# Performance work log

Measured on AMD Instinct MI355X. Metric: run time of the kernel, lower is better.

Reference implementation:

```python
import jax, jax.numpy as jnp
import numpy as np
import math

B, S, H = 2, 2048, 4096
NH, HD, KVH = 32, 128, 8
GROUPS = NH // KVH  # repeat_kv n_rep
BASE = 10000.0
TRAINING_SEQLEN = 8192
BASE_SEQLEN = 8192


def _rope_cos_sin(s):
    # RotaryEmbedding.forward: seq_len = max(s, training_seqlen); NTK-alpha scaled base; mscale
    seq_len = max(s, TRAINING_SEQLEN)
    context_value = math.log(seq_len / BASE_SEQLEN, 2) + 1
    ntk_alpha = max(2 ** math.ceil(context_value) - 1, 1)
    scale = seq_len / TRAINING_SEQLEN
    mscale = 1.0 if scale <= 1 else 0.1 * math.log(scale) + 1.0
    base = BASE * ntk_alpha ** (HD / (HD - 2))
    inv_freq = 1.0 / base ** (np.arange(0, HD, 2, dtype=np.float32) / HD)
    t = np.arange(seq_len, dtype=np.float32)
    freqs = np.outer(t, inv_freq)          # [seq_len, HD/2]
    emb = np.concatenate([freqs, freqs], axis=-1)  # [seq_len, HD]
    return jnp.asarray(mscale * np.cos(emb)[:s]), jnp.asarray(mscale * np.sin(emb)[:s])


def _rotate_half(x):
    x1, x2 = jnp.split(x, 2, axis=-1)
    return jnp.concatenate([-x2, x1], axis=-1)


def setup_inputs() -> dict:
    key = jax.random.key(0)
    ks = jax.random.split(key, 5)
    hidden_states = jax.random.normal(ks[0], (B, S, H), jnp.float32)
    residual = jax.random.normal(ks[1], (B, S, H), jnp.float32)
    causal = jnp.triu(jnp.ones((S, S), dtype=bool), k=1)  # True = masked (masked_fill semantics)
    attention_mask = jnp.broadcast_to(causal[None, None], (B, 1, S, S))
    W_q = jax.random.normal(ks[2], (H, H), jnp.float32) / np.float32(np.sqrt(H))
    W_kv = jax.random.normal(ks[3], (H, 2 * KVH * HD), jnp.float32) / np.float32(np.sqrt(H))
    W_dense = jax.random.normal(ks[4], (H, H), jnp.float32) / np.float32(np.sqrt(H))
    b_dense = jnp.zeros((H,), jnp.float32)
    return dict(hidden_states=hidden_states, residual=residual, attention_mask=attention_mask,
                W_q=W_q, W_kv=W_kv, W_dense=W_dense, b_dense=b_dense)


def reference(hidden_states, residual, attention_mask, W_q, W_kv, W_dense, b_dense):
    # QKV projections (Linear, no bias for query/key_value)
    q = (hidden_states @ W_q).reshape(B, S, NH, HD)            # [B,S,NH,HD]
    kvp = (hidden_states @ W_kv).reshape(B, S, KVH, 2 * HD)
    k, v = kvp[..., :HD], kvp[..., HD:]                        # [B,S,KVH,HD]
    # rotary (NTK-scaled), applied identically to q and k
    cos, sin = _rope_cos_sin(S)
    cos = cos[None, :, None, :]
    sin = sin[None, :, None, :]
    q = q * cos + _rotate_half(q) * sin
    k = k * cos + _rotate_half(k) * sin
    # repeat_kv: each kv head repeated GROUPS times consecutively
    k = jnp.repeat(k, GROUPS, axis=2)                          # [B,S,NH,HD]
    v = jnp.repeat(v, GROUPS, axis=2)
    # scaled dot-product attention with causal mask
    scores = jnp.einsum('bqhd,bkhd->bhqk', q, k) * (1.0 / np.float32(np.sqrt(HD)))
    scores = jnp.where(attention_mask, jnp.finfo(scores.dtype).min, scores)
    probs = jax.nn.softmax(scores, axis=-1)                    # attention_dropout=0 (eval)
    ctx = jnp.einsum('bhqk,bkhd->bqhd', probs, v).reshape(B, S, H)
    # dense (with bias) + dropout_add residual (dropout inactive in eval)
    out = ctx @ W_dense + b_dense
    return residual + out
```

## Files before the change

kernel.cpp:

```cpp
#include <hip/hip_runtime.h>
#include <hip/hip_bf16.h>


#define BB   2
#define SS   2048
#define HH   4096
#define NHH  32
#define HDD  128
#define KVHH 8

typedef unsigned short u16;
typedef __attribute__((ext_vector_type(8))) short  short8;
typedef __attribute__((ext_vector_type(4))) float  floatx4;

#define AS1 __attribute__((address_space(1)))
#define AS3 __attribute__((address_space(3)))

__device__ __forceinline__ void gll16(const void* g, void* l) {
    __builtin_amdgcn_global_load_lds((const AS1 unsigned int*)g,
                                     (AS3 unsigned int*)l, 16, 0, 0);
}
__device__ __forceinline__ float b2f(u16 x) {
    union { unsigned int u; float f; } c; c.u = ((unsigned int)x) << 16; return c.f;
}
__device__ __forceinline__ u16 f2b(float f) {
    union { float f; unsigned int u; } c; c.f = f;
    unsigned int r = 0x7FFFu + ((c.u >> 16) & 1u);
    return (u16)((c.u + r) >> 16);
}

__global__ __launch_bounds__(256)
void cvt_kernel(const float* __restrict__ X, u16* __restrict__ Y, int n4) {
    int i = blockIdx.x * 256 + threadIdx.x;
    if (i >= n4) return;
    float4 v = *(const float4*)(X + (size_t)i * 4);
    size_t o = (size_t)i * 4;
    Y[o + 0] = f2b(v.x); Y[o + 1] = f2b(v.y);
    Y[o + 2] = f2b(v.z); Y[o + 3] = f2b(v.w);
}

__global__ __launch_bounds__(256) void rope_table(float* __restrict__ ct,
                                                  float* __restrict__ st) {
    int idx = blockIdx.x * 256 + threadIdx.x;
    if (idx >= SS * 64) return;
    int s = idx >> 6, i = idx & 63;
    double inv = pow(10000.0, -(double)(2 * i) / 128.0);
    double f = (double)s * inv;
    ct[idx] = (float)cos(f);
    st[idx] = (float)sin(f);
}

__global__ __launch_bounds__(256) void wt_kernel(const float* __restrict__ W,
                                                 u16* __restrict__ WT,
                                                 int R, int C) {
    __shared__ u16 t[64 * 65];
    int tcols = C >> 6;
    int ty = blockIdx.x / tcols, tx = blockIdx.x % tcols;
    int r0 = ty * 64, c0 = tx * 64;
    for (int idx = threadIdx.x; idx < 4096; idx += 256) {
        int r = idx >> 6, c = idx & 63;
        t[r * 65 + c] = f2b(W[(size_t)(r0 + r) * C + c0 + c]);
    }
    __syncthreads();
    for (int idx = threadIdx.x; idx < 4096; idx += 256) {
        int c = idx >> 6, r = idx & 63;
        WT[(size_t)(c0 + c) * R + r0 + r] = t[r * 65 + c];
    }
}

__global__ __launch_bounds__(256, 2)
void gemm_bt(const u16* __restrict__ A, const u16* __restrict__ BT,
             u16* __restrict__ C, float* __restrict__ Cf,
             int M, int N, int K,
             const float* __restrict__ bias, const float* __restrict__ resid) {
    __shared__ u16 sA[128 * 32];
    __shared__ u16 sB[128 * 32];
    const int tid = threadIdx.x;
    const int wave = tid >> 6, lane = tid & 63;
    const int m0 = blockIdx.y * 128, n0 = blockIdx.x * 128;
    const int wm = (wave >> 1) * 64, wn = (wave & 1) * 64;
    const int srow = lane >> 2, scol = (lane & 3) * 8;
    const int frow = lane & 15, fquad = lane >> 4;
    const int fk = fquad * 8;

    const floatx4 fz = {0.f, 0.f, 0.f, 0.f};
    floatx4 acc[4][4];
#pragma unroll
    for (int i = 0; i < 4; ++i)
#pragma unroll
        for (int j = 0; j < 4; ++j) acc[i][j] = fz;

    for (int kt = 0; kt < K; kt += 32) {
#pragma unroll
        for (int j = 0; j < 2; ++j) {
            int rb = (wave + j * 4) * 16;
            gll16(A  + (size_t)(m0 + rb + srow) * K + kt + scol, &sA[rb * 32]);
            gll16(BT + (size_t)(n0 + rb + srow) * K + kt + scol, &sB[rb * 32]);
        }
        __syncthreads();
        short8 af[4];
#pragma unroll
        for (int i = 0; i < 4; ++i)
            af[i] = *(const short8*)&sA[(wm + i * 16 + frow) * 32 + fk];
#pragma unroll
        for (int jn = 0; jn < 4; ++jn) {
            short8 bfr = *(const short8*)&sB[(wn + jn * 16 + frow) * 32 + fk];
#pragma unroll
            for (int i = 0; i < 4; ++i)
                acc[i][jn] = __builtin_amdgcn_mfma_f32_16x16x32_bf16(
                    af[i], bfr, acc[i][jn], 0, 0, 0);
        }
        __syncthreads();
    }
#pragma unroll
    for (int i = 0; i < 4; ++i) {
#pragma unroll
        for (int jn = 0; jn < 4; ++jn) {
            int col = n0 + wn + jn * 16 + frow;
            float bv = bias ? bias[col] : 0.f;
#pragma unroll
            for (int r = 0; r < 4; ++r) {
                int row = m0 + wm + i * 16 + fquad * 4 + r;
                float v = acc[i][jn][r] + bv;
                if (Cf) {
                    if (resid) v += resid[(size_t)row * N + col];
                    Cf[(size_t)row * N + col] = v;
                } else {
                    C[(size_t)row * N + col] = f2b(v);
                }
            }
        }
    }
}

__global__ __launch_bounds__(256)
void rope_apply(u16* __restrict__ Qb, u16* __restrict__ KVb,
                const float* __restrict__ ct, const float* __restrict__ st) {
    int gid = blockIdx.x * 256 + threadIdx.x;
    int row = gid >> 6, d = gid & 63;
    const int nq = BB * SS * NHH;
    u16* p;
    int s;
    if (row < nq) {
        s = (row / NHH) % SS;
        p = Qb + (size_t)row * HDD;
    } else {
        int r2 = row - nq;
        s = (r2 / KVHH) % SS;
        p = KVb + (size_t)r2 * 256;
    }
    float c = ct[s * 64 + d], sn = st[s * 64 + d];
    float x0 = b2f(p[d]), x1 = b2f(p[d + 64]);
    p[d]      = f2b(x0 * c - x1 * sn);
    p[d + 64] = f2b(x1 * c + x0 * sn);
}

__global__ __launch_bounds__(256)
void vt_kernel(const u16* __restrict__ KVb, u16* __restrict__ VT) {
    __shared__ u16 t[64 * 130];
    int bid = blockIdx.x;
    int bk = bid >> 5;
    int s0 = (bid & 31) * 64;
    int b = bk >> 3, kvh = bk & 7;
    for (int idx = threadIdx.x; idx < 64 * 128; idx += 256) {
        int si = idx >> 7, d = idx & 127;
        t[si * 130 + d] =
            KVb[((size_t)((b * SS + s0 + si) * KVHH + kvh)) * 256 + 128 + d];
    }
    __syncthreads();
    for (int idx = threadIdx.x; idx < 64 * 128; idx += 256) {
        int d = idx >> 6, sj = idx & 63;
        VT[((size_t)(bk * HDD + d)) * SS + s0 + sj] = t[sj * 130 + d];
    }
}

__global__ __launch_bounds__(256, 3)
void attn(const u16* __restrict__ Q, const u16* __restrict__ KV,
          const u16* __restrict__ VT, u16* __restrict__ CTX) {
    __shared__ u16 smem[25600];
    u16* sK  = smem;
    u16* sVT = smem + 8192;
    u16* sP  = smem + 16384;

    const int tid = threadIdx.x;
    const int wave = tid >> 6, lane = tid & 63;
    const int frow = lane & 15, fquad = lane >> 4;
    const int bid = blockIdx.x;
    const int qt = 15 - (bid >> 6);
    const int b = (bid >> 5) & 1;
    const int h = bid & 31;
    const int kvh = h >> 2;
    const int q0 = qt * 128;

    {
        const int srow4 = lane >> 4;
        const int chunk = lane & 15;
#pragma unroll
        for (int j = 0; j < 8; ++j) {
            int rb = (j * 4 + wave) * 4;
            int sc = chunk ^ ((rb + srow4) & 7);
            gll16(Q + ((size_t)((b * SS + q0 + rb + srow4) * NHH + h)) * HDD + sc * 8,
                  &smem[rb * 128]);
        }
    }
    __syncthreads();
    short8 qf[2][4];
#pragma unroll
    for (int mi = 0; mi < 2; ++mi)
#pragma unroll
        for (int ds = 0; ds < 4; ++ds)
            qf[mi][ds] = *(const short8*)
                &smem[(wave * 32 + mi * 16 + frow) * 128 +
                      ((ds * 4 + fquad) ^ (frow & 7)) * 8];
    __syncthreads();

    const floatx4 fz = {0.f, 0.f, 0.f, 0.f};
    floatx4 o[2][8];
#pragma unroll
    for (int mi = 0; mi < 2; ++mi)
#pragma unroll
        for (int dn = 0; dn < 8; ++dn) o[mi][dn] = fz;
    float mrow[2][4], lrow[2][4];
#pragma unroll
    for (int mi = 0; mi < 2; ++mi)
#pragma unroll
        for (int r = 0; r < 4; ++r) { mrow[mi][r] = -1e30f; lrow[mi][r] = 0.f; }

    const float scale = 0.08838834764831845f;
    const int nt = 2 * (qt + 1);
    for (int t = 0; t < nt; ++t) {
        const int k0 = t * 64;
        {
            const int srow4 = lane >> 4, ch16 = lane & 15;
#pragma unroll
            for (int j = 0; j < 4; ++j) {
                int rb = (j * 4 + wave) * 4;
                int sc = ch16 ^ ((rb + srow4) & 7);
                gll16(KV + ((size_t)((b * SS + k0 + rb + srow4) * KVHH + kvh)) * 256 + sc * 8,
                      &sK[rb * 128]);
            }
            const int srow8 = lane >> 3, ch8 = lane & 7;
#pragma unroll
            for (int j = 0; j < 4; ++j) {
                int rb = (j * 4 + wave) * 8;
                int sc = ch8 ^ ((rb + srow8) & 7);
                gll16(VT + ((size_t)((b * KVHH + kvh) * HDD + rb + srow8)) * SS + k0 + sc * 8,
                      &sVT[rb * 64]);
            }
        }
        __syncthreads();

        floatx4 sc[2][4];
#pragma unroll
        for (int mi = 0; mi < 2; ++mi)
#pragma unroll
            for (int ni = 0; ni < 4; ++ni) sc[mi][ni] = fz;
#pragma unroll
        for (int ds = 0; ds < 4; ++ds) {
#pragma unroll
            for (int ni = 0; ni < 4; ++ni) {
                short8 kf = *(const short8*)
                    &sK[(ni * 16 + frow) * 128 +
                        ((ds * 4 + fquad) ^ (frow & 7)) * 8];
                sc[0][ni] = __builtin_amdgcn_mfma_f32_16x16x32_bf16(
                    qf[0][ds], kf, sc[0][ni], 0, 0, 0);
                sc[1][ni] = __builtin_amdgcn_mfma_f32_16x16x32_bf16(
                    qf[1][ds], kf, sc[1][ni], 0, 0, 0);
            }
        }

        const bool dgt = (t >= 2 * qt);
#pragma unroll
        for (int mi = 0; mi < 2; ++mi) {
#pragma unroll
            for (int r = 0; r < 4; ++r) {
                int qg = q0 + wave * 32 + mi * 16 + fquad * 4 + r;
                float mx = -1e30f;
#pragma unroll
                for (int ni = 0; ni < 4; ++ni) {
                    float v = sc[mi][ni][r] * scale;
                    if (dgt) {
                        int kg = k0 + ni * 16 + frow;
                        if (kg > qg) v = -1e30f;
                    }
                    sc[mi][ni][r] = v;
                    mx = fmaxf(mx, v);
                }
                mx = fmaxf(mx, __shfl_xor(mx, 1));
                mx = fmaxf(mx, __shfl_xor(mx, 2));
                mx = fmaxf(mx, __shfl_xor(mx, 4));
                mx = fmaxf(mx, __shfl_xor(mx, 8));
                float mold = mrow[mi][r];
                float mnew = fmaxf(mold, mx);
                float alpha = __expf(mold - mnew);
                mrow[mi][r] = mnew;
                float rs = 0.f;
#pragma unroll
                for (int ni = 0; ni < 4; ++ni) {
                    float pv = __expf(sc[mi][ni][r] - mnew);
                    sc[mi][ni][r] = pv;
                    rs += pv;
                }
                rs += __shfl_xor(rs, 1);
                rs += __shfl_xor(rs, 2);
                rs += __shfl_xor(rs, 4);
                rs += __shfl_xor(rs, 8);
                lrow[mi][r] = lrow[mi][r] * alpha + rs;
#pragma unroll
                for (int dn = 0; dn < 8; ++dn) o[mi][dn][r] *= alpha;
            }
        }

#pragma unroll
        for (int mi = 0; mi < 2; ++mi)
#pragma unroll
            for (int ni = 0; ni < 4; ++ni)
#pragma unroll
                for (int r = 0; r < 4; ++r)
                    sP[(wave * 32 + mi * 16 + fquad * 4 + r) * 72 + ni * 16 + frow] =
                        f2b(sc[mi][ni][r]);
        asm volatile("s_waitcnt lgkmcnt(0)" ::: "memory");

#pragma unroll
        for (int ks = 0; ks < 2; ++ks) {
            short8 pf0 = *(const short8*)
                &sP[(wave * 32 + frow) * 72 + ks * 32 + fquad * 8];
            short8 pf1 = *(const short8*)
                &sP[(wave * 32 + 16 + frow) * 72 + ks * 32 + fquad * 8];
#pragma unroll
            for (int dn = 0; dn < 8; ++dn) {
                short8 vf = *(const short8*)
                    &sVT[(dn * 16 + frow) * 64 +
                         ((ks * 4 + fquad) ^ (frow & 7)) * 8];
                o[0][dn] = __builtin_amdgcn_mfma_f32_16x16x32_bf16(pf0, vf, o[0][dn], 0, 0, 0);
                o[1][dn] = __builtin_amdgcn_mfma_f32_16x16x32_bf16(pf1, vf, o[1][dn], 0, 0, 0);
            }
        }
        __syncthreads();
    }

#pragma unroll
    for (int mi = 0; mi < 2; ++mi) {
#pragma unroll
        for (int r = 0; r < 4; ++r) {
            float inv = 1.f / lrow[mi][r];
            int qg = q0 + wave * 32 + mi * 16 + fquad * 4 + r;
            size_t base = ((size_t)(b * SS + qg) * NHH + h) * HDD;
#pragma unroll
            for (int dn = 0; dn < 8; ++dn)
                CTX[base + dn * 16 + frow] = f2b(o[mi][dn][r] * inv);
        }
    }
}

extern "C" void kernel_launch(void* const* d_in, const int* in_sizes, int n_in,
                              void* d_out, int out_size, void* d_ws, size_t ws_size,
                              hipStream_t stream) {
    const float* hidden = (const float*)d_in[0];
    const float* resid  = (const float*)d_in[1];
    const float* Wq  = (const float*)d_in[3];
    const float* Wkv = (const float*)d_in[4];
    const float* Wd  = (const float*)d_in[5];
    const float* bd  = (const float*)d_in[6];
    float* out = (float*)d_out;

    char* ws = (char*)d_ws;
    u16*   hsb = (u16*)(ws);
    u16*   Qb  = (u16*)(ws + ((size_t)32 << 20));
    u16*   KVb = (u16*)(ws + ((size_t)64 << 20));
    u16*   T1  = (u16*)(ws + ((size_t)80 << 20));
    u16*   VTb = (u16*)(ws + ((size_t)112 << 20));
    float* ct  = (float*)(ws + ((size_t)120 << 20));
    float* st  = (float*)(ws + ((size_t)120 << 20) + ((size_t)512 << 10));

    const int M = BB * SS;

    rope_table<<<512, 256, 0, stream>>>(ct, st);
    cvt_kernel<<<(M * HH / 4 + 255) / 256, 256, 0, stream>>>(hidden, hsb, M * HH / 4);

    wt_kernel<<<4096, 256, 0, stream>>>(Wq, T1, HH, HH);
    gemm_bt<<<dim3(32, 32), 256, 0, stream>>>(hsb, T1, Qb, nullptr, M, HH, HH,
                                              nullptr, nullptr);
    wt_kernel<<<2048, 256, 0, stream>>>(Wkv, T1, HH, 2 * KVHH * HDD);
    gemm_bt<<<dim3(16, 32), 256, 0, stream>>>(hsb, T1, KVb, nullptr,
                                              M, 2 * KVHH * HDD, HH,
                                              nullptr, nullptr);

    rope_apply<<<(BB * SS * (NHH + KVHH) * 64) / 256, 256, 0, stream>>>(Qb, KVb, ct, st);
    vt_kernel<<<BB * KVHH * (SS / 64), 256, 0, stream>>>(KVb, VTb);

    attn<<<BB * 16 * NHH, 256, 0, stream>>>(Qb, KVb, VTb, Qb);

    wt_kernel<<<4096, 256, 0, stream>>>(Wd, T1, HH, HH);
    gemm_bt<<<dim3(32, 32), 256, 0, stream>>>(Qb, T1, nullptr, out, M, HH, HH,
                                              bd, resid);
}
```

Before: 984.8 us.

## Register-prefetch K/V tiles in attention, lazy softmax rescale, vectorize rope

The attention loop now prefetches the next K and V^T tiles from global memory into registers while the current tile is computed, replacing the direct global-to-LDS loads. This is meant to hide load latency behind the MFMA work. Softmax rescaling of the output accumulators is skipped unless some row max grows by more than 8, and s_setprio is raised around the MFMA blocks. The rope kernel handles four elements per thread with vector loads and stores. The trade-offs are higher register pressure and an extra register-to-LDS copy per tile.

```diff
diff --git a/kernel.cpp b/kernel.cpp
--- a/kernel.cpp
+++ b/kernel.cpp
@@ -11,6 +11,7 @@
 
 typedef unsigned short u16;
 typedef __attribute__((ext_vector_type(8))) short  short8;
+typedef __attribute__((ext_vector_type(4))) short  short4b;
 typedef __attribute__((ext_vector_type(4))) float  floatx4;
 
 #define AS1 __attribute__((address_space(1)))
@@ -137,7 +138,7 @@
 void rope_apply(u16* __restrict__ Qb, u16* __restrict__ KVb,
                 const float* __restrict__ ct, const float* __restrict__ st) {
     int gid = blockIdx.x * 256 + threadIdx.x;
-    int row = gid >> 6, d = gid & 63;
+    int row = gid >> 4, d4 = (gid & 15) * 4;
     const int nq = BB * SS * NHH;
     u16* p;
     int s;
@@ -149,10 +150,22 @@
         s = (r2 / KVHH) % SS;
         p = KVb + (size_t)r2 * 256;
     }
-    float c = ct[s * 64 + d], sn = st[s * 64 + d];
-    float x0 = b2f(p[d]), x1 = b2f(p[d + 64]);
-    p[d]      = f2b(x0 * c - x1 * sn);
-    p[d + 64] = f2b(x1 * c + x0 * sn);
+    float4 c  = *(const float4*)(ct + s * 64 + d4);
+    float4 sn = *(const float4*)(st + s * 64 + d4);
+    short4b lo = *(short4b*)(p + d4);
+    short4b hi = *(short4b*)(p + d4 + 64);
+    short4b nlo, nhi;
+    float x0, x1;
+    x0 = b2f((u16)lo[0]); x1 = b2f((u16)hi[0]);
+    nlo[0] = (short)f2b(x0 * c.x - x1 * sn.x); nhi[0] = (short)f2b(x1 * c.x + x0 * sn.x);
+    x0 = b2f((u16)lo[1]); x1 = b2f((u16)hi[1]);
+    nlo[1] = (short)f2b(x0 * c.y - x1 * sn.y); nhi[1] = (short)f2b(x1 * c.y + x0 * sn.y);
+    x0 = b2f((u16)lo[2]); x1 = b2f((u16)hi[2]);
+    nlo[2] = (short)f2b(x0 * c.z - x1 * sn.z); nhi[2] = (short)f2b(x1 * c.z + x0 * sn.z);
+    x0 = b2f((u16)lo[3]); x1 = b2f((u16)hi[3]);
+    nlo[3] = (short)f2b(x0 * c.w - x1 * sn.w); nhi[3] = (short)f2b(x1 * c.w + x0 * sn.w);
+    *(short4b*)(p + d4)      = nlo;
+    *(short4b*)(p + d4 + 64) = nhi;
 }
 
 __global__ __launch_bounds__(256)
@@ -226,35 +239,50 @@
 #pragma unroll
         for (int r = 0; r < 4; ++r) { mrow[mi][r] = -1e30f; lrow[mi][r] = 0.f; }
 
+    const int ksrow = lane >> 4, kch = lane & 15;
+    const int vsrow = lane >> 3, vch = lane & 7;
+
+    short8 kreg[4], vreg[4];
+    auto LOAD = [&](int t) {
+        const int k0 = t * 64;
+#pragma unroll
+        for (int j = 0; j < 4; ++j) {
+            int krow = (j * 4 + wave) * 4 + ksrow;
+            int ksc = kch ^ (krow & 7);
+            kreg[j] = *(const short8*)
+                (KV + ((size_t)((b * SS + k0 + krow) * KVHH + kvh)) * 256 + ksc * 8);
+            int vrow = (j * 4 + wave) * 8 + vsrow;
+            int vsc = vch ^ (vrow & 7);
+            vreg[j] = *(const short8*)
+                (VT + ((size_t)((b * KVHH + kvh) * HDD + vrow)) * SS + k0 + vsc * 8);
+        }
+    };
+    auto WRITE = [&]() {
+#pragma unroll
+        for (int j = 0; j < 4; ++j) {
+            int krow = (j * 4 + wave) * 4 + ksrow;
+            *(short8*)&sK[krow * 128 + kch * 8] = kreg[j];
+            int vrow = (j * 4 + wave) * 8 + vsrow;
+            *(short8*)&sVT[vrow * 64 + vch * 8] = vreg[j];
+        }
+    };
+
     const float scale = 0.08838834764831845f;
     const int nt = 2 * (qt + 1);
+    LOAD(0);
     for (int t = 0; t < nt; ++t) {
+        WRITE();
+        __syncthreads();
+        if (t + 1 < nt) LOAD(t + 1);
+
         const int k0 = t * 64;
-        {
-            const int srow4 = lane >> 4, ch16 = lane & 15;
-#pragma unroll
-            for (int j = 0; j < 4; ++j) {
-                int rb = (j * 4 + wave) * 4;
-                int sc = ch16 ^ ((rb + srow4) & 7);
-                gll16(KV + ((size_t)((b * SS + k0 + rb + srow4) * KVHH + kvh)) * 256 + sc * 8,
-                      &sK[rb * 128]);
-            }
-            const int srow8 = lane >> 3, ch8 = lane & 7;
-#pragma unroll
-            for (int j = 0; j < 4; ++j) {
-                int rb = (j * 4 + wave) * 8;
-                int sc = ch8 ^ ((rb + srow8) & 7);
-                gll16(VT + ((size_t)((b * KVHH + kvh) * HDD + rb + srow8)) * SS + k0 + sc * 8,
-                      &sVT[rb * 64]);
-            }
-        }
-        __syncthreads();
 
         floatx4 sc[2][4];
 #pragma unroll
         for (int mi = 0; mi < 2; ++mi)
 #pragma unroll
             for (int ni = 0; ni < 4; ++ni) sc[mi][ni] = fz;
+        __builtin_amdgcn_s_setprio(1);
 #pragma unroll
         for (int ds = 0; ds < 4; ++ds) {
 #pragma unroll
@@ -268,14 +296,16 @@
                     qf[1][ds], kf, sc[1][ni], 0, 0, 0);
             }
         }
+        __builtin_amdgcn_s_setprio(0);
 
         const bool dgt = (t >= 2 * qt);
+        float mx[2][4];
 #pragma unroll
         for (int mi = 0; mi < 2; ++mi) {
 #pragma unroll
             for (int r = 0; r < 4; ++r) {
                 int qg = q0 + wave * 32 + mi * 16 + fquad * 4 + r;
-                float mx = -1e30f;
+                float m = -1e30f;
 #pragma unroll
                 for (int ni = 0; ni < 4; ++ni) {
                     float v = sc[mi][ni][r] * scale;
@@ -284,20 +314,45 @@
                         if (kg > qg) v = -1e30f;
                     }
                     sc[mi][ni][r] = v;
-                    mx = fmaxf(mx, v);
+                    m = fmaxf(m, v);
                 }
-                mx = fmaxf(mx, __shfl_xor(mx, 1));
-                mx = fmaxf(mx, __shfl_xor(mx, 2));
-                mx = fmaxf(mx, __shfl_xor(mx, 4));
-                mx = fmaxf(mx, __shfl_xor(mx, 8));
-                float mold = mrow[mi][r];
-                float mnew = fmaxf(mold, mx);
-                float alpha = __expf(mold - mnew);
-                mrow[mi][r] = mnew;
+                m = fmaxf(m, __shfl_xor(m, 1));
+                m = fmaxf(m, __shfl_xor(m, 2));
+                m = fmaxf(m, __shfl_xor(m, 4));
+                m = fmaxf(m, __shfl_xor(m, 8));
+                mx[mi][r] = m;
+            }
+        }
+        bool grow = false;
+#pragma unroll
+        for (int mi = 0; mi < 2; ++mi)
+#pragma unroll
+            for (int r = 0; r < 4; ++r)
+                grow |= (mx[mi][r] > mrow[mi][r] + 8.f);
+        if (__any(grow)) {
+#pragma unroll
+            for (int mi = 0; mi < 2; ++mi) {
+#pragma unroll
+                for (int r = 0; r < 4; ++r) {
+                    float mold = mrow[mi][r];
+                    float mnew = fmaxf(mold, mx[mi][r]);
+                    float alpha = __expf(mold - mnew);
+                    mrow[mi][r] = mnew;
+                    lrow[mi][r] *= alpha;
+#pragma unroll
+                    for (int dn = 0; dn < 8; ++dn) o[mi][dn][r] *= alpha;
+                }
+            }
+        }
+#pragma unroll
+        for (int mi = 0; mi < 2; ++mi) {
+#pragma unroll
+            for (int r = 0; r < 4; ++r) {
+                float mm = mrow[mi][r];
                 float rs = 0.f;
 #pragma unroll
                 for (int ni = 0; ni < 4; ++ni) {
-                    float pv = __expf(sc[mi][ni][r] - mnew);
+                    float pv = __expf(sc[mi][ni][r] - mm);
                     sc[mi][ni][r] = pv;
                     rs += pv;
                 }
@@ -305,9 +360,7 @@
                 rs += __shfl_xor(rs, 2);
                 rs += __shfl_xor(rs, 4);
                 rs += __shfl_xor(rs, 8);
-                lrow[mi][r] = lrow[mi][r] * alpha + rs;
-#pragma unroll
-                for (int dn = 0; dn < 8; ++dn) o[mi][dn][r] *= alpha;
+                lrow[mi][r] += rs;
             }
         }
 
@@ -321,6 +374,7 @@
                         f2b(sc[mi][ni][r]);
         asm volatile("s_waitcnt lgkmcnt(0)" ::: "memory");
 
+        __builtin_amdgcn_s_setprio(1);
 #pragma unroll
         for (int ks = 0; ks < 2; ++ks) {
             short8 pf0 = *(const short8*)
@@ -336,6 +390,7 @@
                 o[1][dn] = __builtin_amdgcn_mfma_f32_16x16x32_bf16(pf1, vf, o[1][dn], 0, 0, 0);
             }
         }
+        __builtin_amdgcn_s_setprio(0);
         __syncthreads();
     }
 
@@ -386,7 +441,7 @@
                                               M, 2 * KVHH * HDD, HH,
                                               nullptr, nullptr);
 
-    rope_apply<<<(BB * SS * (NHH + KVHH) * 64) / 256, 256, 0, stream>>>(Qb, KVb, ct, st);
+    rope_apply<<<(BB * SS * (NHH + KVHH) * 16) / 256, 256, 0, stream>>>(Qb, KVb, ct, st);
     vt_kernel<<<BB * KVHH * (SS / 64), 256, 0, stream>>>(KVb, VTb);
 
     attn<<<BB * 16 * NHH, 256, 0, stream>>>(Qb, KVb, VTb, Qb);
```

New measurement: 1.192 ms. +21.0%, slower.
